# Performance work log

Hardware: AMD Instinct MI355X
Metric: run time of the kernel (lower is better)

## Reference

```python
import jax, jax.numpy as jnp
import numpy as np

T, B, I, H = 512, 32, 512, 512

def setup_inputs() -> dict:
    key = jax.random.key(0)
    k1, k2, k3 = jax.random.split(key, 3)
    x = jax.random.normal(k1, (T, B, I), dtype=jnp.float32)
    h0 = jnp.zeros((B, H), dtype=jnp.float32)
    W_ih = jax.random.normal(k2, (3 * H, I), dtype=jnp.float32) * (1.0 / np.sqrt(H))
    # diagonal recurrent weights, one vector per gate (r, z, n), uniform(-1, 1)
    w_hh = jax.random.uniform(k3, (3, H), dtype=jnp.float32, minval=-1.0, maxval=1.0)
    return {"x": x, "h0": h0, "W_ih": W_ih, "w_hh": w_hh}

def reference(x, h0, W_ih, w_hh):
    # Precompute input-side gate pre-activations for all timesteps: (T, B, 3H)
    gx = jnp.einsum('tbi,gi->tbg', x, W_ih)
    xr, xz, xn = jnp.split(gx, 3, axis=-1)  # each (T, B, H)
    w_r, w_z, w_n = w_hh[0], w_hh[1], w_hh[2]  # each (H,)

    def step(h, g):
        gr, gz, gn = g
        r = jax.nn.sigmoid(gr + w_r * h)
        z = jax.nn.sigmoid(gz + w_z * h)
        n = jnp.tanh(gn + r * (w_n * h))
        h_new = (1.0 - z) * n + z * h
        return h_new, h_new

    h_last, out = jax.lax.scan(step, h0, (xr, xz, xn))
    # out: (T, B, H) all hidden states; h_last: (1, B, H) final state (GRU convention)
    return out, h_last[None, :, :]
```

## Files before the change

### kernel.cpp

```cpp
#include <hip/hip_runtime.h>
#include <hip/hip_bf16.h>
#include <stdint.h>

#define T_DIM 512
#define B_DIM 32
#define K_DIM 512
#define H_DIM 512
#define N_DIM 1536
#define M_DIM 16384

typedef __bf16 bf16_t;
typedef bf16_t bf16x8 __attribute__((ext_vector_type(8)));
typedef float floatx4 __attribute__((ext_vector_type(4)));

#define LOG2E 1.442695041f
#define TWO_LOG2E 2.885390082f

__device__ __forceinline__ unsigned int f2bf_bits(float f) {
  uint32_t u = __builtin_bit_cast(uint32_t, f);
  u += 0x7FFFu + ((u >> 16) & 1u);
  return u >> 16;
}

__global__ void convert_both_kernel(const float* __restrict__ x,
                                    unsigned short* __restrict__ xb,
                                    const float* __restrict__ W,
                                    unsigned short* __restrict__ Wb) {
  int bid = blockIdx.x;
  const float* src;
  unsigned short* dst;
  int i;
  if (bid < 4096) {
    i = (bid * 256 + threadIdx.x) * 8;
    src = x + i;
    dst = xb + i;
  } else {
    i = ((bid - 4096) * 256 + threadIdx.x) * 8;
    int n = i >> 9;
    int k = i & 511;
    int p6 = n / 6;
    int sub = n - p6 * 6;
    int hodd = (sub >= 3) ? 1 : 0;
    int g = sub - hodd * 3;
    int h = p6 * 2 + hodd;
    src = W + ((g << 9) + h) * 512 + k;
    dst = Wb + i;
  }
  const float4* p = (const float4*)src;
  float4 f0 = p[0];
  float4 f1 = p[1];
  uint4 v;
  v.x = f2bf_bits(f0.x) | (f2bf_bits(f0.y) << 16);
  v.y = f2bf_bits(f0.z) | (f2bf_bits(f0.w) << 16);
  v.z = f2bf_bits(f1.x) | (f2bf_bits(f1.y) << 16);
  v.w = f2bf_bits(f1.z) | (f2bf_bits(f1.w) << 16);
  *(uint4*)dst = v;
}

__global__ __launch_bounds__(512, 4) void gemm_bf16_kernel(
    const unsigned short* __restrict__ A, const unsigned short* __restrict__ Bm,
    _Float16* __restrict__ C) {
  __shared__ bf16_t smem[24576];
  const int tid = threadIdx.x;
  const int lane = tid & 63;
  const int w = tid >> 6;
  const int tileM = blockIdx.x * 256;
  const int tileN = blockIdx.y * 128;
  const int waveM = w & 3;
  const int waveN = w >> 2;
  const int lm = lane & 15;
  const int lg = lane >> 4;

  floatx4 acc[4][4] = {};

  for (int k0 = 0; k0 < K_DIM; k0 += 64) {
#pragma unroll
    for (int g = 0; g < 4; ++g) {
      int s = g * 512 + tid;
      int row = s >> 3;
      int kc = (s & 7) ^ (row & 7);
      bf16_t* la = smem + (g * 512 + w * 64) * 8;
      const unsigned short* ga = A + (size_t)(tileM + row) * K_DIM + k0 + kc * 8;
      __builtin_amdgcn_global_load_lds(
          (const __attribute__((address_space(1))) unsigned int*)ga,
          (__attribute__((address_space(3))) unsigned int*)la, 16, 0, 0);
    }
#pragma unroll
    for (int g = 0; g < 2; ++g) {
      int s = g * 512 + tid;
      int row = s >> 3;
      int kc = (s & 7) ^ (row & 7);
      bf16_t* lb = smem + 16384 + (g * 512 + w * 64) * 8;
      const unsigned short* gb = Bm + (size_t)(tileN + row) * K_DIM + k0 + kc * 8;
      __builtin_amdgcn_global_load_lds(
          (const __attribute__((address_space(1))) unsigned int*)gb,
          (__attribute__((address_space(3))) unsigned int*)lb, 16, 0, 0);
    }
    __syncthreads();

#pragma unroll
    for (int ks = 0; ks < 2; ++ks) {
      bf16x8 af[4], bfg[4];
#pragma unroll
      for (int i = 0; i < 4; ++i) {
        int row = waveM * 64 + i * 16 + lm;
        int c = ks * 4 + lg;
        af[i] = *(const bf16x8*)(smem + row * 64 + (c ^ (row & 7)) * 8);
      }
#pragma unroll
      for (int j = 0; j < 4; ++j) {
        int row = waveN * 64 + j * 16 + lm;
        int c = ks * 4 + lg;
        bfg[j] = *(const bf16x8*)(smem + 16384 + row * 64 + (c ^ (row & 7)) * 8);
      }
#pragma unroll
      for (int i = 0; i < 4; ++i)
#pragma unroll
        for (int j = 0; j < 4; ++j)
          acc[i][j] = __builtin_amdgcn_mfma_f32_16x16x32_bf16(af[i], bfg[j],
                                                              acc[i][j], 0, 0, 0);
    }
    __syncthreads();
  }

  _Float16* ep = (_Float16*)smem + w * 2048;
  const int q = lm;
  const int rgrp = lane >> 4;
  const size_t crow0 = (size_t)(tileM + waveM * 64);
  const int ccol = tileN + waveN * 64 + q * 4;
#pragma unroll
  for (int p = 0; p < 2; ++p) {
#pragma unroll
    for (int il = 0; il < 2; ++il) {
      const int i = 2 * p + il;
#pragma unroll
      for (int j = 0; j < 4; ++j) {
        const int cl = lm + j * 16;
        const int sub = (tileN + waveN * 64 + cl) % 6;
        const float scl = (sub == 2 || sub == 5) ? TWO_LOG2E : -LOG2E;
#pragma unroll
        for (int r = 0; r < 4; ++r) {
          int rl = (lane >> 4) * 4 + r + 16 * il;
          ep[rl * 64 + cl] = (_Float16)(scl * acc[i][j][r]);
        }
      }
    }
#pragma unroll
    for (int k = 0; k < 8; ++k) {
      int rl = rgrp + 4 * k;
      uint2 v = *(const uint2*)(ep + rl * 64 + q * 4);
      *(uint2*)(C + (crow0 + p * 32 + rl) * N_DIM + ccol) = v;
    }
  }
}

__global__ __launch_bounds__(64) void indgru_scan_kernel(
    const _Float16* __restrict__ gx, const float* __restrict__ h0,
    const float* __restrict__ w_hh, float* __restrict__ out,
    float* __restrict__ hlast) {
  const int idx = blockIdx.x * 64 + threadIdx.x;
  const int b = idx >> 9;
  const int h = idx & (H_DIM - 1);
  const float wr = -LOG2E * w_hh[h];
  const float wz = -LOG2E * w_hh[H_DIM + h];
  const float wn = TWO_LOG2E * w_hh[2 * H_DIM + h];
  const int sh = (h & 1) << 4;
  float hv = h0[idx];

  const char* base = (const char*)(gx + (size_t)b * N_DIM + (h >> 1) * 6) + ((h & 1) << 2);
  float* outp = out + (size_t)b * H_DIM + h;

  constexpr int D = 32;
  constexpr size_t TSTRIDE = (size_t)B_DIM * N_DIM * sizeof(_Float16);
  uint2 pq[D];
#pragma unroll
  for (int t = 0; t < D; ++t)
    pq[t] = *(const uint2*)(base + (size_t)t * TSTRIDE);

  auto cvt16 = [](uint32_t bits) {
    return (float)__builtin_bit_cast(_Float16, (unsigned short)bits);
  };

  for (int t0 = 0; t0 < T_DIM - D; t0 += D) {
#pragma unroll
    for (int s = 0; s < D; ++s) {
      const int t = t0 + s;
      uint2 q = pq[s];
      pq[s] = *(const uint2*)(base + (size_t)(t + D) * TSTRIDE);
      asm volatile("" ::: "memory");
      uint64_t v = (((uint64_t)q.y << 32) | q.x) >> sh;
      float gr = cvt16((uint32_t)v);
      float gz = cvt16((uint32_t)(v >> 16));
      float gn = cvt16((uint32_t)(v >> 32));
      float ar = fmaf(wr, hv, gr);
      float az = fmaf(wz, hv, gz);
      float t1 = wn * hv;
      float er = __builtin_amdgcn_exp2f(ar);
      float ez = __builtin_amdgcn_exp2f(az);
      float r = __builtin_amdgcn_rcpf(1.0f + er);
      float z = __builtin_amdgcn_rcpf(1.0f + ez);
      float en = __builtin_amdgcn_exp2f(fmaf(r, t1, gn));
      float u = __builtin_amdgcn_rcpf(1.0f + en);
      float n = fmaf(-2.0f, u, 1.0f);
      float zh = z * hv;
      float omz = 1.0f - z;
      hv = fmaf(n, omz, zh);
      outp[(size_t)t * (B_DIM * H_DIM)] = hv;
    }
  }
#pragma unroll
  for (int s = 0; s < D; ++s) {
    const int t = T_DIM - D + s;
    uint2 q = pq[s];
    uint64_t v = (((uint64_t)q.y << 32) | q.x) >> sh;
    float gr = cvt16((uint32_t)v);
    float gz = cvt16((uint32_t)(v >> 16));
    float gn = cvt16((uint32_t)(v >> 32));
    float ar = fmaf(wr, hv, gr);
    float az = fmaf(wz, hv, gz);
    float t1 = wn * hv;
    float er = __builtin_amdgcn_exp2f(ar);
    float ez = __builtin_amdgcn_exp2f(az);
    float r = __builtin_amdgcn_rcpf(1.0f + er);
    float z = __builtin_amdgcn_rcpf(1.0f + ez);
    float en = __builtin_amdgcn_exp2f(fmaf(r, t1, gn));
    float u = __builtin_amdgcn_rcpf(1.0f + en);
    float n = fmaf(-2.0f, u, 1.0f);
    float zh = z * hv;
    float omz = 1.0f - z;
    hv = fmaf(n, omz, zh);
    outp[(size_t)t * (B_DIM * H_DIM)] = hv;
  }
  hlast[idx] = hv;
}

extern "C" void kernel_launch(void* const* d_in, const int* in_sizes, int n_in,
                              void* d_out, int out_size, void* d_ws, size_t ws_size,
                              hipStream_t stream) {
  const float* x    = (const float*)d_in[0];
  const float* h0   = (const float*)d_in[1];
  const float* W_ih = (const float*)d_in[2];
  const float* w_hh = (const float*)d_in[3];

  float* out = (float*)d_out;
  float* hlast = out + (size_t)T_DIM * B_DIM * H_DIM;

  char* ws = (char*)d_ws;
  unsigned short* xb = (unsigned short*)ws;
  unsigned short* Wb = (unsigned short*)(ws + 16777216);
  _Float16* gx = (_Float16*)(ws + 16777216 + 1572864);

  convert_both_kernel<<<4480, 256, 0, stream>>>(x, xb, W_ih, Wb);

  dim3 grid(M_DIM / 256, N_DIM / 128);
  gemm_bf16_kernel<<<grid, 512, 0, stream>>>(xb, Wb, gx);

  indgru_scan_kernel<<<256, 64, 0, stream>>>(gx, h0, w_hh, out, hlast);
}
```

Baseline: 152.2 us.

## Enlarge GEMM tile to 256x256 with double-buffered LDS prefetch pipeline

The GEMM tile grows from 256x128 to 256x256, and LDS becomes double-buffered at 128 KB so the next K-slice of A and B is loaded while MFMAs run on the current one. Explicit vmcnt/lgkmcnt waits, split barriers and s_setprio replace the per-iteration syncthreads. The aim is more reuse of each loaded fragment and hidden global-load latency. In exchange, occupancy drops to fewer blocks per CU and the grid halves to 384 blocks, which may leave CUs underfilled.

```diff
diff --git a/kernel.cpp b/kernel.cpp
--- a/kernel.cpp
+++ b/kernel.cpp
@@ -57,79 +57,101 @@
   *(uint4*)dst = v;
 }
 
-__global__ __launch_bounds__(512, 4) void gemm_bf16_kernel(
+__global__ __launch_bounds__(512, 2) void gemm_bf16_kernel(
     const unsigned short* __restrict__ A, const unsigned short* __restrict__ Bm,
     _Float16* __restrict__ C) {
-  __shared__ bf16_t smem[24576];
+  __shared__ bf16_t smem[65536];
   const int tid = threadIdx.x;
   const int lane = tid & 63;
   const int w = tid >> 6;
   const int tileM = blockIdx.x * 256;
-  const int tileN = blockIdx.y * 128;
-  const int waveM = w & 3;
-  const int waveN = w >> 2;
+  const int tileN = blockIdx.y * 256;
+  const int waveM = w >> 2;
+  const int waveN = w & 3;
   const int lm = lane & 15;
   const int lg = lane >> 4;
 
-  floatx4 acc[4][4] = {};
-
-  for (int k0 = 0; k0 < K_DIM; k0 += 64) {
-#pragma unroll
-    for (int g = 0; g < 4; ++g) {
-      int s = g * 512 + tid;
-      int row = s >> 3;
+  floatx4 acc[8][4] = {};
+
+  auto stage = [&](const unsigned short* __restrict__ G, int tileR, int kt,
+                   int half, int bOfs) {
+#pragma unroll
+    for (int q = 0; q < 2; ++q) {
+      int s = q * 512 + tid;
+      int row = half * 128 + (s >> 3);
       int kc = (s & 7) ^ (row & 7);
-      bf16_t* la = smem + (g * 512 + w * 64) * 8;
-      const unsigned short* ga = A + (size_t)(tileM + row) * K_DIM + k0 + kc * 8;
+      bf16_t* dst = smem + (kt & 1) * 32768 + bOfs + (half * 1024 + s) * 8;
+      const unsigned short* gsrc =
+          G + (size_t)(tileR + row) * K_DIM + kt * 64 + kc * 8;
       __builtin_amdgcn_global_load_lds(
-          (const __attribute__((address_space(1))) unsigned int*)ga,
-          (__attribute__((address_space(3))) unsigned int*)la, 16, 0, 0);
-    }
-#pragma unroll
-    for (int g = 0; g < 2; ++g) {
-      int s = g * 512 + tid;
-      int row = s >> 3;
-      int kc = (s & 7) ^ (row & 7);
-      bf16_t* lb = smem + 16384 + (g * 512 + w * 64) * 8;
-      const unsigned short* gb = Bm + (size_t)(tileN + row) * K_DIM + k0 + kc * 8;
-      __builtin_amdgcn_global_load_lds(
-          (const __attribute__((address_space(1))) unsigned int*)gb,
-          (__attribute__((address_space(3))) unsigned int*)lb, 16, 0, 0);
-    }
-    __syncthreads();
-
-#pragma unroll
-    for (int ks = 0; ks < 2; ++ks) {
-      bf16x8 af[4], bfg[4];
-#pragma unroll
-      for (int i = 0; i < 4; ++i) {
-        int row = waveM * 64 + i * 16 + lm;
-        int c = ks * 4 + lg;
-        af[i] = *(const bf16x8*)(smem + row * 64 + (c ^ (row & 7)) * 8);
+          (const __attribute__((address_space(1))) unsigned int*)gsrc,
+          (__attribute__((address_space(3))) unsigned int*)dst, 16, 0, 0);
+    }
+  };
+
+  stage(A, tileM, 0, 0, 0);
+  stage(A, tileM, 0, 1, 0);
+  stage(Bm, tileN, 0, 0, 16384);
+  stage(Bm, tileN, 0, 1, 16384);
+
+#pragma unroll
+  for (int t = 0; t < 8; ++t) {
+    const bf16_t* As = smem + (t & 1) * 32768;
+    const bf16_t* Bs = As + 16384;
+    if (t + 1 < 8) {
+      stage(A, tileM, t + 1, 0, 0);
+      stage(A, tileM, t + 1, 1, 0);
+      asm volatile("s_waitcnt vmcnt(4)" ::: "memory");
+    } else {
+      asm volatile("s_waitcnt vmcnt(0)" ::: "memory");
+    }
+    __builtin_amdgcn_s_barrier();
+
+    bf16x8 bfr[4];
+#pragma unroll
+    for (int kk = 0; kk < 2; ++kk) {
+#pragma unroll
+      for (int rh = 0; rh < 2; ++rh) {
+        bf16x8 afr[4];
+        const int c = kk * 4 + lg;
+#pragma unroll
+        for (int i = 0; i < 4; ++i) {
+          int row = waveM * 128 + (rh * 4 + i) * 16 + lm;
+          afr[i] = *(const bf16x8*)(As + row * 64 + ((c ^ (row & 7)) << 3));
+        }
+        if (rh == 0) {
+#pragma unroll
+          for (int j = 0; j < 4; ++j) {
+            int row = waveN * 64 + j * 16 + lm;
+            bfr[j] = *(const bf16x8*)(Bs + row * 64 + ((c ^ (row & 7)) << 3));
+          }
+        }
+        if (kk == 0 && rh == 0 && t + 1 < 8) {
+          stage(Bm, tileN, t + 1, 0, 16384);
+          stage(Bm, tileN, t + 1, 1, 16384);
+        }
+        __builtin_amdgcn_s_barrier();
+        asm volatile("s_waitcnt lgkmcnt(0)" ::: "memory");
+        __builtin_amdgcn_s_setprio(1);
+#pragma unroll
+        for (int i = 0; i < 4; ++i)
+#pragma unroll
+          for (int j = 0; j < 4; ++j)
+            acc[rh * 4 + i][j] = __builtin_amdgcn_mfma_f32_16x16x32_bf16(
+                afr[i], bfr[j], acc[rh * 4 + i][j], 0, 0, 0);
+        __builtin_amdgcn_s_setprio(0);
+        __builtin_amdgcn_s_barrier();
       }
-#pragma unroll
-      for (int j = 0; j < 4; ++j) {
-        int row = waveN * 64 + j * 16 + lm;
-        int c = ks * 4 + lg;
-        bfg[j] = *(const bf16x8*)(smem + 16384 + row * 64 + (c ^ (row & 7)) * 8);
-      }
-#pragma unroll
-      for (int i = 0; i < 4; ++i)
-#pragma unroll
-        for (int j = 0; j < 4; ++j)
-          acc[i][j] = __builtin_amdgcn_mfma_f32_16x16x32_bf16(af[i], bfg[j],
-                                                              acc[i][j], 0, 0, 0);
-    }
-    __syncthreads();
+    }
   }
 
   _Float16* ep = (_Float16*)smem + w * 2048;
   const int q = lm;
   const int rgrp = lane >> 4;
-  const size_t crow0 = (size_t)(tileM + waveM * 64);
+  const size_t crow0 = (size_t)(tileM + waveM * 128);
   const int ccol = tileN + waveN * 64 + q * 4;
 #pragma unroll
-  for (int p = 0; p < 2; ++p) {
+  for (int p = 0; p < 4; ++p) {
 #pragma unroll
     for (int il = 0; il < 2; ++il) {
       const int i = 2 * p + il;
@@ -185,10 +207,10 @@
 #pragma unroll
     for (int s = 0; s < D; ++s) {
       const int t = t0 + s;
-      uint2 q = pq[s];
+      uint2 qv = pq[s];
       pq[s] = *(const uint2*)(base + (size_t)(t + D) * TSTRIDE);
       asm volatile("" ::: "memory");
-      uint64_t v = (((uint64_t)q.y << 32) | q.x) >> sh;
+      uint64_t v = (((uint64_t)qv.y << 32) | qv.x) >> sh;
       float gr = cvt16((uint32_t)v);
       float gz = cvt16((uint32_t)(v >> 16));
       float gn = cvt16((uint32_t)(v >> 32));
@@ -211,8 +233,8 @@
 #pragma unroll
   for (int s = 0; s < D; ++s) {
     const int t = T_DIM - D + s;
-    uint2 q = pq[s];
-    uint64_t v = (((uint64_t)q.y << 32) | q.x) >> sh;
+    uint2 qv = pq[s];
+    uint64_t v = (((uint64_t)qv.y << 32) | qv.x) >> sh;
     float gr = cvt16((uint32_t)v);
     float gz = cvt16((uint32_t)(v >> 16));
     float gn = cvt16((uint32_t)(v >> 32));
@@ -252,7 +274,7 @@
 
   convert_both_kernel<<<4480, 256, 0, stream>>>(x, xb, W_ih, Wb);
 
-  dim3 grid(M_DIM / 256, N_DIM / 128);
+  dim3 grid(M_DIM / 256, N_DIM / 256);
   gemm_bf16_kernel<<<grid, 512, 0, stream>>>(xb, Wb, gx);
 
   indgru_scan_kernel<<<256, 64, 0, stream>>>(gx, h0, w_hh, out, hlast);
```

After: 155.4 us. 2.1% more time.
